# Performance work log

Measured on AMD Instinct MI355X. Metric: run time of the kernel, lower is better.

The kernel has to match this reference:

```python
import jax, jax.numpy as jnp
import numpy as np

T, B, S, D = 512, 32, 512, 512
EPS = 1e-6  # LayerNorm eps


def _ln(x, g, b):
    m = jnp.mean(x, axis=-1, keepdims=True)
    v = jnp.mean((x - m) ** 2, axis=-1, keepdims=True)
    return g * (x - m) * jax.lax.rsqrt(v + EPS) + b


def setup_inputs() -> dict:
    key = jax.random.key(0)
    ks = jax.random.split(key, 10)
    sc = 1.0 / np.sqrt(D).astype(np.float32)
    return {
        "prev_layer": jax.random.normal(ks[0], (T, B, D), jnp.float32),
        "hidden": jax.random.normal(ks[1], (B, D), jnp.float32),
        "enc_output": jax.random.normal(ks[2], (B, S, D), jnp.float32),
        "memory_length": jax.random.randint(ks[3], (B,), 1, S + 1),
        # nn.Linear weights stored as [in, out] (transposed torch layout)
        "W_in": jax.random.normal(ks[4], (D, 3 * D), jnp.float32) * sc,
        "W_enc": jax.random.normal(ks[5], (D, D), jnp.float32) * sc,
        "W_attn_in": jax.random.normal(ks[6], (D, D), jnp.float32) * sc,
        "W_hidden": jax.random.normal(ks[7], (D, D), jnp.float32) * sc,
        "W_ctx": jax.random.normal(ks[8], (D, D), jnp.float32) * sc,
        # LayerNorm gains/biases (5 LNs)
        "g_pre": jnp.ones((3 * D,), jnp.float32), "b_pre": jnp.zeros((3 * D,), jnp.float32),
        "g_enc": jnp.ones((D,), jnp.float32), "b_enc": jnp.zeros((D,), jnp.float32),
        "g_attn": jnp.ones((D,), jnp.float32), "b_attn": jnp.zeros((D,), jnp.float32),
        "g_h": jnp.ones((D,), jnp.float32), "b_h": jnp.zeros((D,), jnp.float32),
        "g_c": jnp.ones((D,), jnp.float32), "b_c": jnp.zeros((D,), jnp.float32),
    }


def reference(prev_layer, hidden, enc_output, W_in, W_enc, W_attn_in, W_hidden,
              W_ctx, g_pre, b_pre, g_enc, b_enc, g_attn, b_attn, g_h, b_h,
              g_c, b_c, memory_length):
    d = prev_layer.shape[-1]
    sqrt_d = jnp.sqrt(jnp.asarray(d, prev_layer.dtype))
    # dropout is identity in eval mode
    preact = _ln(prev_layer @ W_in, g_pre, b_pre)          # [T,B,3D]
    pctx = _ln(enc_output @ W_enc, g_enc, b_enc)           # [B,S,D]
    z, h_gate, pl_t = jnp.split(preact, 3, axis=-1)
    z = jax.nn.sigmoid(z)
    h_gate = jax.nn.sigmoid(h_gate)

    # SRU-style linear recurrence: s_t = (1-z_t)*s_{t-1} + z_t*pl_t
    def step(h, zp):
        z_t, p_t = zp
        s = (1.0 - z_t) * h + z_t * p_t
        return s, s

    hidden_last, ss = jax.lax.scan(step, hidden, (z, pl_t))  # ss: [T,B,D]

    attn_in = _ln(ss @ W_attn_in, g_attn, b_attn)            # [T,B,D]
    align = jnp.einsum('tbd,bsd->bts', attn_in, pctx)        # [B,T,S]
    mask = jnp.arange(pctx.shape[1])[None, :] < memory_length[:, None]  # [B,S]
    align = jnp.where(mask[:, None, :], align, -jnp.inf)
    av = jax.nn.softmax(align / sqrt_d, axis=-1)             # [B,T,S]
    c = jnp.einsum('bts,bsd->tbd', av, pctx)                 # [T,B,D]
    attn_out = c / sqrt_d

    trans = _ln(ss @ W_hidden, g_h, b_h) + _ln(attn_out @ W_ctx, g_c, b_c)
    out = jnp.tanh(trans)
    out = (1.0 - h_gate) * out + h_gate * prev_layer         # [T,B,D]
    p_attn = jnp.transpose(av, (1, 0, 2))                    # [T,B,S]
    return out, hidden_last, p_attn
```

## Files before the change

kernel.cpp:

```cpp
#include <hip/hip_runtime.h>
#include <hip/hip_bf16.h>
#include <cmath>

#define T_ 512
#define B_ 32
#define S_ 512
#define D_ 512
#define NCH 16
#define CT (T_ / NCH)
static constexpr float LN_EPS = 1e-6f;
static constexpr float RSQRT_D = 0.044194173824159216f;

typedef __attribute__((ext_vector_type(8))) __bf16 bf16x8;
typedef __attribute__((ext_vector_type(4))) float f32x4;

struct __align__(8) bfx4 { __hip_bfloat16 x, y, z, w; };
struct __align__(16) u16x8 { unsigned short h[8]; };

__device__ __forceinline__ void g2l16(const void* g, void* l) {
    __builtin_amdgcn_global_load_lds(
        (const __attribute__((address_space(1))) unsigned int*)g,
        (__attribute__((address_space(3))) unsigned int*)l, 16, 0, 0);
}

__device__ __forceinline__ float xr_sum16(float v) {
    v += __shfl_xor(v, 1); v += __shfl_xor(v, 2);
    v += __shfl_xor(v, 4); v += __shfl_xor(v, 8); return v;
}
__device__ __forceinline__ float xr_max16(float v) {
    v = fmaxf(v, __shfl_xor(v, 1)); v = fmaxf(v, __shfl_xor(v, 2));
    v = fmaxf(v, __shfl_xor(v, 4)); v = fmaxf(v, __shfl_xor(v, 8)); return v;
}

__device__ __forceinline__ float sigmoidf_(float x) {
    return 1.f / (1.f + __expf(-x));
}
__device__ __forceinline__ float sigmoid_fast(float x) {
    return __fdividef(1.f, 1.f + __expf(-x));
}
__device__ __forceinline__ float tanh_fast(float x) {
    return 1.f - __fdividef(2.f, __expf(2.f * x) + 1.f);
}
__device__ __forceinline__ float bfu(unsigned short u) {
    unsigned int v = ((unsigned int)u) << 16;
    return __uint_as_float(v);
}

__device__ __forceinline__ void g128_body(
    const __hip_bfloat16* __restrict__ A, long ldaE,
    const __hip_bfloat16* __restrict__ Bw,
    __hip_bfloat16* __restrict__ out, long outStrideB,
    float2* __restrict__ part, int partMul, int partBase,
    float scale, int bx, int by)
{
    __shared__ char smem[32768];
    const int m0 = by * 128, n0 = bx * 128;
    const int tid = threadIdx.x, lane = tid & 63, w = tid >> 6;
    const int wm = (w >> 1) * 64, wn = (w & 1) * 64;
    const int srow = lane >> 2, skB = (lane & 3) * 16;
    const int q = lane >> 4, c = lane & 15;

    f32x4 acc[4][4];
#pragma unroll
    for (int i = 0; i < 4; i++)
#pragma unroll
        for (int j = 0; j < 4; j++) acc[i][j] = (f32x4)(0.0f);

    const char* ga0 = (const char*)(A + (long)(m0 + w * 16 + srow) * ldaE) + skB;
    const char* ga1 = (const char*)(A + (long)(m0 + (w + 4) * 16 + srow) * ldaE) + skB;
    const char* gb0 = (const char*)(Bw + (long)(n0 + w * 16 + srow) * 512) + skB;
    const char* gb1 = (const char*)(Bw + (long)(n0 + (w + 4) * 16 + srow) * 512) + skB;
    char* la0 = smem + w * 1024 + lane * 16;
    char* la1 = smem + (w + 4) * 1024 + lane * 16;
    char* lb0 = smem + 8192 + w * 1024 + lane * 16;
    char* lb1 = smem + 8192 + (w + 4) * 1024 + lane * 16;
    const char* Ar = smem + (wm + c) * 64 + q * 16;
    const char* Br = smem + 8192 + (wn + c) * 64 + q * 16;

    g2l16(ga0, la0);
    g2l16(ga1, la1);
    g2l16(gb0, lb0);
    g2l16(gb1, lb1);
    __syncthreads();

#pragma unroll
    for (int kk = 0; kk < 16; kk++) {
        const int cb = (kk & 1) << 14;
        const int nb = cb ^ 16384;
        if (kk < 15) {
            const long kb = (long)(kk + 1) * 64;
            g2l16(ga0 + kb, la0 + nb);
            g2l16(ga1 + kb, la1 + nb);
            g2l16(gb0 + kb, lb0 + nb);
            g2l16(gb1 + kb, lb1 + nb);
        }
        bf16x8 af[4], bfr[4];
#pragma unroll
        for (int i = 0; i < 4; i++) {
            af[i] = *(const bf16x8*)(Ar + cb + i * 1024);
            bfr[i] = *(const bf16x8*)(Br + cb + i * 1024);
        }
#pragma unroll
        for (int i = 0; i < 4; i++)
#pragma unroll
            for (int j = 0; j < 4; j++)
                acc[i][j] = __builtin_amdgcn_mfma_f32_16x16x32_bf16(
                    af[i], bfr[j], acc[i][j], 0, 0, 0);
        __syncthreads();
    }

    if (part) {
        float2* sred = (float2*)smem;
#pragma unroll
        for (int i = 0; i < 4; i++)
#pragma unroll
            for (int r = 0; r < 4; r++) {
                float s = 0.f, qq = 0.f;
#pragma unroll
                for (int j = 0; j < 4; j++) {
                    float v = acc[i][j][r] * scale; s += v; qq += v * v;
                }
                s = xr_sum16(s); qq = xr_sum16(qq);
                if (c == 0) sred[(wm + i * 16 + q * 4 + r) * 2 + (w & 1)] =
                    make_float2(s, qq);
            }
        __syncthreads();
        if ((w & 1) == 0 && c == 0) {
#pragma unroll
            for (int i = 0; i < 4; i++)
#pragma unroll
                for (int r = 0; r < 4; r++) {
                    int row = wm + i * 16 + q * 4 + r;
                    float2 a = sred[row * 2], b2 = sred[row * 2 + 1];
                    part[(long)bx * 16384 + (long)(m0 + row) * partMul + partBase] =
                        make_float2(a.x + b2.x, a.y + b2.y);
                }
        }
        __syncthreads();
    }

    for (int p = 0; p < 2; p++) {
        if ((w >> 1) == p) {
#pragma unroll
            for (int i = 0; i < 4; i++)
#pragma unroll
                for (int j = 0; j < 4; j++)
#pragma unroll
                    for (int r = 0; r < 4; r++) {
                        int row = i * 16 + q * 4 + r;
                        int col = wn + j * 16 + c;
                        ((__hip_bfloat16*)smem)[row * 128 + col] =
                            __float2bfloat16(acc[i][j][r] * scale);
                    }
        }
        __syncthreads();
#pragma unroll
        for (int rnd = 0; rnd < 4; rnd++) {
            int row = rnd * 16 + (tid >> 4);
            int ch = tid & 15;
            uint4 v = *(const uint4*)(smem + row * 256 + ch * 16);
            long grow = m0 + p * 64 + row;
            *(uint4*)((char*)out + grow * outStrideB + (long)n0 * 2 + ch * 16) = v;
        }
        __syncthreads();
    }
}

__global__ __launch_bounds__(256) void g128(
    const __hip_bfloat16* __restrict__ A, long ldaE,
    const __hip_bfloat16* __restrict__ Bw, long bStrideZ,
    __hip_bfloat16* __restrict__ out, long outStrideB,
    float2* __restrict__ part, float scale, int swizzle)
{
    int bx, by, pmul = 1, pbase = 0;
    if (gridDim.z > 1) {
        bx = blockIdx.x; by = blockIdx.y;
        A += (long)blockIdx.z * 512;
        Bw += (long)blockIdx.z * bStrideZ;
        out += (long)blockIdx.z * 512;
        pmul = 32; pbase = blockIdx.z;
    } else if (swizzle) {
        const int nwg = gridDim.x * gridDim.y;
        const int lin = blockIdx.y * gridDim.x + blockIdx.x;
        const int cpx = nwg >> 3;
        const int swz = (lin & 7) * cpx + (lin >> 3);
        bx = swz % gridDim.x; by = swz / gridDim.x;
    } else { bx = blockIdx.x; by = blockIdx.y; }
    g128_body(A, ldaE, Bw, out, outStrideB, part, pmul, pbase, scale, bx, by);
}

__global__ __launch_bounds__(256) void g128mid(
    const __hip_bfloat16* __restrict__ encb,
    const __hip_bfloat16* __restrict__ ssb,
    const __hip_bfloat16* __restrict__ WE2,
    const __hip_bfloat16* __restrict__ WAH,
    __hip_bfloat16* __restrict__ E2, __hip_bfloat16* __restrict__ C2,
    float2* __restrict__ partA, float2* __restrict__ partB)
{
    const int lin = blockIdx.x;
    const int swz = (lin & 7) * 256 + (lin >> 3);
    const __hip_bfloat16 *A, *Bw;
    __hip_bfloat16* out;
    float2* part;
    int local;
    if (swz < 1024) { A = encb; Bw = WE2; out = E2; part = partA; local = swz; }
    else { A = ssb; Bw = WAH; out = C2; part = partB; local = swz - 1024; }
    const int bx = local & 7, by = local >> 3;
    g128_body(A, 512, Bw, out, 2048, part, 1, 0, 1.f, bx, by);
}

#define RC_BUF 34816
__device__ __forceinline__ void rows_core32_lds(
    const __hip_bfloat16* A, long lda,
    const __hip_bfloat16* B, long ldb,
    char* smem, f32x4 (&acc)[2][8])
{
    const int tid = threadIdx.x, lane = tid & 63, w = tid >> 6;
#pragma unroll
    for (int m = 0; m < 2; m++)
#pragma unroll
        for (int j = 0; j < 8; j++) acc[m][j] = (f32x4)(0.0f);

    const char* ga = (const char*)(A + (long)(w * 16 + (lane >> 2)) * lda) + (lane & 3) * 16;
    char* la = smem + w * 1024 + lane * 16;
    const char* gb = (const char*)(B + (long)(w * 128 + (lane >> 2)) * ldb) + (lane & 3) * 16;
    char* lb = smem + 2048 + w * 8192 + lane * 16;
    const long ldbB16 = (long)ldb * 32;
    const char* Ar = smem + (lane & 15) * 64 + (lane >> 4) * 16;
    const char* Br = smem + 2048 + (w * 128 + (lane & 15)) * 64 + (lane >> 4) * 16;

    if (w < 2) g2l16(ga, la);
#pragma unroll
    for (int s = 0; s < 8; s++) g2l16(gb + s * ldbB16, lb + s * 1024);
    __syncthreads();

#pragma unroll
    for (int kk = 0; kk < 16; kk++) {
        const int cb = (kk & 1) * RC_BUF;
        const int nb = ((kk & 1) ^ 1) * RC_BUF;
        if (kk < 15) {
            const long kb = (long)(kk + 1) * 64;
            if (w < 2) g2l16(ga + kb, la + nb);
#pragma unroll
            for (int s = 0; s < 8; s++)
                g2l16(gb + kb + s * ldbB16, lb + nb + s * 1024);
        }
        bf16x8 af[2], bfr[8];
#pragma unroll
        for (int m = 0; m < 2; m++) af[m] = *(const bf16x8*)(Ar + cb + m * 1024);
#pragma unroll
        for (int j = 0; j < 8; j++) bfr[j] = *(const bf16x8*)(Br + cb + j * 1024);
#pragma unroll
        for (int m = 0; m < 2; m++)
#pragma unroll
            for (int j = 0; j < 8; j++)
                acc[m][j] = __builtin_amdgcn_mfma_f32_16x16x32_bf16(
                    af[m], bfr[j], acc[m][j], 0, 0, 0);
        __syncthreads();
    }
}

__global__ __launch_bounds__(256, 2) void gemm_attn(
    const __hip_bfloat16* __restrict__ attninC2,
    const __hip_bfloat16* __restrict__ pctxb,
    const int* __restrict__ mlen,
    float* __restrict__ pattn, __hip_bfloat16* __restrict__ softb)
{
    __shared__ char smem[69632];
    const int b = blockIdx.z;
    const long t0 = (long)blockIdx.y * 32;
    f32x4 acc[2][8];
    rows_core32_lds(attninC2 + (long)b * 1024 + t0 * 32768, 32768,
                    pctxb + (long)b * 262144, 512, smem, acc);

    const int tid = threadIdx.x, lane = tid & 63, w = tid >> 6;
    const int q = lane >> 4, c = lane & 15;
    const int len = mlen[b];
    float* sred = (float*)smem;

#pragma unroll
    for (int m = 0; m < 2; m++)
#pragma unroll
        for (int r = 0; r < 4; r++) {
            float mx = -INFINITY;
#pragma unroll
            for (int j = 0; j < 8; j++) {
                int col = w * 128 + j * 16 + c;
                float v = acc[m][j][r] * RSQRT_D;
                acc[m][j][r] = v;
                if (col < len) mx = fmaxf(mx, v);
            }
            mx = xr_max16(mx);
            if (c == 0) sred[(m * 16 + q * 4 + r) * 4 + w] = mx;
        }
    __syncthreads();
    float rmax[2][4];
#pragma unroll
    for (int m = 0; m < 2; m++)
#pragma unroll
        for (int r = 0; r < 4; r++) {
            int row = m * 16 + q * 4 + r;
            rmax[m][r] = fmaxf(fmaxf(sred[row * 4], sred[row * 4 + 1]),
                               fmaxf(sred[row * 4 + 2], sred[row * 4 + 3]));
        }
    __syncthreads();
#pragma unroll
    for (int m = 0; m < 2; m++)
#pragma unroll
        for (int r = 0; r < 4; r++) {
            float s = 0.f;
#pragma unroll
            for (int j = 0; j < 8; j++) {
                int col = w * 128 + j * 16 + c;
                float e = (col < len) ? __expf(acc[m][j][r] - rmax[m][r]) : 0.f;
                acc[m][j][r] = e; s += e;
            }
            s = xr_sum16(s);
            if (c == 0) sred[(m * 16 + q * 4 + r) * 4 + w] = s;
        }
    __syncthreads();
    float rinv[2][4];
#pragma unroll
    for (int m = 0; m < 2; m++)
#pragma unroll
        for (int r = 0; r < 4; r++) {
            int row = m * 16 + q * 4 + r;
            rinv[m][r] = 1.f / (sred[row * 4] + sred[row * 4 + 1] +
                                sred[row * 4 + 2] + sred[row * 4 + 3]);
        }
    __syncthreads();

#pragma unroll
    for (int m = 0; m < 2; m++)
#pragma unroll
        for (int j = 0; j < 8; j++)
#pragma unroll
            for (int r = 0; r < 4; r++) {
                int row = m * 16 + q * 4 + r;
                int col = w * 128 + j * 16 + c;
                float p = acc[m][j][r] * rinv[m][r];
                acc[m][j][r] = p;
                pattn[((t0 + row) * 32 + b) * 512 + col] = p;
                ((__hip_bfloat16*)smem)[row * 512 + col] = __float2bfloat16(p);
            }
    __syncthreads();
#pragma unroll
    for (int rnd = 0; rnd < 8; rnd++) {
        int row = rnd * 4 + w;
        uint4 v = *(const uint4*)(smem + row * 1024 + lane * 16);
        *(uint4*)((char*)softb + ((t0 + row) * 32 + b) * 1024 + lane * 16) = v;
    }
}

__global__ __launch_bounds__(256) void stats4(
    const float2* __restrict__ part, float2* __restrict__ st)
{
    int r = blockIdx.x * 256 + threadIdx.x;
    float s = 0.f, qq = 0.f;
#pragma unroll
    for (int cb = 0; cb < 4; cb++) {
        float2 v = part[(long)cb * 16384 + r]; s += v.x; qq += v.y;
    }
    float m = s * (1.f / 512);
    float rs = rsqrtf(qq * (1.f / 512) - m * m + LN_EPS);
    st[r] = make_float2(m, rs);
}

__global__ __launch_bounds__(256) void ln_apply_s(
    __hip_bfloat16* __restrict__ x,
    const float2* __restrict__ st,
    const float* __restrict__ g, const float* __restrict__ bb)
{
    int i = blockIdx.x * 256 + threadIdx.x;
    int row = i >> 6;
    int c0 = (i & 63) * 8;
    float2 s = st[row];
    char* p = (char*)x + (long)row * 2048 + (long)(i & 63) * 16;
    u16x8 v = *(const u16x8*)p;
    float4 g0 = *(const float4*)(g + c0), g1 = *(const float4*)(g + c0 + 4);
    float4 b0 = *(const float4*)(bb + c0), b1 = *(const float4*)(bb + c0 + 4);
    float gv[8] = {g0.x, g0.y, g0.z, g0.w, g1.x, g1.y, g1.z, g1.w};
    float bv[8] = {b0.x, b0.y, b0.z, b0.w, b1.x, b1.y, b1.z, b1.w};
#pragma unroll
    for (int k = 0; k < 8; k++) {
        float f = (bfu(v.h[k]) - s.x) * s.y * gv[k] + bv[k];
        v.h[k] = __hip_bfloat16_raw(__float2bfloat16(f)).x;
    }
    *(u16x8*)p = v;
}

__global__ __launch_bounds__(256) void midfix(
    const __hip_bfloat16* __restrict__ E2,
    __hip_bfloat16* __restrict__ pctxb, __hip_bfloat16* __restrict__ pwT,
    const float2* __restrict__ st,
    const float* __restrict__ g, const float* __restrict__ bb,
    const float* __restrict__ uv)
{
    const int b = blockIdx.z, d0 = blockIdx.x * 32, s0 = blockIdx.y * 32;
    __shared__ __hip_bfloat16 t[32][34];
    const int tx = threadIdx.x & 31, ty = threadIdx.x >> 5;
    const float gv = g[d0 + tx], bv = bb[d0 + tx];
    const float ud = uv[d0 + tx], vd = uv[512 + d0 + tx];
#pragma unroll
    for (int i = 0; i < 4; i++) {
        int srow = s0 + ty + i * 8;
        long row = (long)b * 512 + srow;
        float2 s = st[row];
        float pc = __bfloat162float(E2[row * 1024 + d0 + tx]);
        pctxb[row * 512 + d0 + tx] =
            __float2bfloat16((pc - s.x) * s.y * gv + bv);
        float pr = __bfloat162float(E2[row * 1024 + 512 + d0 + tx]);
        t[ty + i * 8][tx] = __float2bfloat16(s.y * pr - s.y * s.x * ud + vd);
    }
    __syncthreads();
#pragma unroll
    for (int i = 0; i < 4; i++)
        pwT[(long)b * 262144 + (long)(d0 + ty + i * 8) * 512 + s0 + tx] =
            t[tx][ty + i * 8];
}

__global__ __launch_bounds__(256) void fin_ep(
    const __hip_bfloat16* __restrict__ h2r,
    const __hip_bfloat16* __restrict__ C2,
    const __hip_bfloat16* __restrict__ preb,
    const float2* __restrict__ st_c, const float2* __restrict__ st_h,
    const float2* __restrict__ st_p,
    const float* __restrict__ g_c, const float* __restrict__ b_c,
    const float* __restrict__ g_h, const float* __restrict__ b_h,
    const float* __restrict__ g_pre, const float* __restrict__ b_pre,
    const float* __restrict__ prev, float* __restrict__ out)
{
    const long m0 = (long)blockIdx.x * 32;
    const int tid = threadIdx.x;
#pragma unroll
    for (int ch = 0; ch < 16; ch++) {
        int f4 = ch * 256 + tid;
        int row = f4 >> 7;
        long rowg = m0 + row;
        int col = (f4 & 127) * 4;
        ushort4 h2 = *(const ushort4*)((const char*)h2r + rowg * 1024 + col * 2);
        ushort4 h1 = *(const ushort4*)((const char*)C2 + rowg * 2048 + 1024 + col * 2);
        ushort4 hr = *(const ushort4*)((const char*)preb + rowg * 3072 + 1024 + col * 2);
        float4 pv = *(const float4*)(prev + rowg * 512 + col);
        float4 gc = *(const float4*)(g_c + col), bc = *(const float4*)(b_c + col);
        float4 gh = *(const float4*)(g_h + col), bh = *(const float4*)(b_h + col);
        float4 gp = *(const float4*)(g_pre + 512 + col);
        float4 bp = *(const float4*)(b_pre + 512 + col);
        float2 sc = st_c[rowg], sh = st_h[rowg], sp = st_p[rowg];
        auto fuse = [&](unsigned short h2u, unsigned short h1u, unsigned short hru,
                        float pvv, float gcv, float bcv, float ghv, float bhv,
                        float gpv, float bpv) -> float {
            float t2 = (bfu(h2u) - sc.x) * sc.y * gcv + bcv;
            float t1 = (bfu(h1u) - sh.x) * sh.y * ghv + bhv;
            float hg = sigmoid_fast((bfu(hru) - sp.x) * sp.y * gpv + bpv);
            return (1.f - hg) * tanh_fast(t1 + t2) + hg * pvv;
        };
        float4 o;
        o.x = fuse(h2.x, h1.x, hr.x, pv.x, gc.x, bc.x, gh.x, bh.x, gp.x, bp.x);
        o.y = fuse(h2.y, h1.y, hr.y, pv.y, gc.y, bc.y, gh.y, bh.y, gp.y, bp.y);
        o.z = fuse(h2.z, h1.z, hr.z, pv.z, gc.z, bc.z, gh.z, bh.z, gp.z, bp.z);
        o.w = fuse(h2.w, h1.w, hr.w, pv.w, gc.w, bc.w, gh.w, bh.w, gp.w, bp.w);
        *(float4*)(out + rowg * 512 + col) = o;
    }
}

__global__ __launch_bounds__(256) void cvt4(
    const float* __restrict__ x, __hip_bfloat16* __restrict__ y, int n4)
{
    int i = blockIdx.x * 256 + threadIdx.x;
    if (i >= n4) return;
    float4 v = ((const float4*)x)[i];
    bfx4 o;
    o.x = __float2bfloat16(v.x); o.y = __float2bfloat16(v.y);
    o.z = __float2bfloat16(v.z); o.w = __float2bfloat16(v.w);
    ((bfx4*)y)[i] = o;
}

__global__ __launch_bounds__(256) void wtrans(
    const float* __restrict__ w0, const float* __restrict__ w1,
    const float* __restrict__ w2, const float* __restrict__ w3,
    const float* __restrict__ w4, __hip_bfloat16* __restrict__ WT,
    __hip_bfloat16* __restrict__ WE2)
{
    int z = blockIdx.z;
    const float* W; __hip_bfloat16* O; int N;
    if (z == 0)      { W = w0; O = WT;                          N = 1536; }
    else if (z == 1) { W = w1; O = WE2;                         N = 512; }
    else if (z == 2) { W = w2; O = WT + 786432 + 262144;        N = 512; }
    else if (z == 3) { W = w3; O = WT + 786432 + 524288;        N = 512; }
    else             { W = w4; O = WT + 786432 + 786432;        N = 512; }
    int n0 = blockIdx.x * 32, k0 = blockIdx.y * 32;
    if (n0 >= N) return;
    __shared__ float t[32][33];
    int tx = threadIdx.x & 31, ty = threadIdx.x >> 5;
#pragma unroll
    for (int i = 0; i < 4; i++)
        t[ty + i * 8][tx] = W[(long)(k0 + ty + i * 8) * N + n0 + tx];
    __syncthreads();
#pragma unroll
    for (int i = 0; i < 4; i++)
        O[(long)(n0 + ty + i * 8) * 512 + k0 + tx] =
            __float2bfloat16(t[tx][ty + i * 8]);
}

__global__ __launch_bounds__(256) void wgscale(
    const __hip_bfloat16* __restrict__ wctxT, const float* __restrict__ g,
    __hip_bfloat16* __restrict__ wgT)
{
    int i = blockIdx.x * 256 + threadIdx.x;
    int d1 = i & 511;
    wgT[i] = __float2bfloat16(__bfloat162float(wctxT[i]) * g[d1]);
}

__global__ __launch_bounds__(256) void uvk(
    const float* __restrict__ Wctx, const float* __restrict__ g,
    const float* __restrict__ b, float* __restrict__ uv)
{
    int d = blockIdx.x * 256 + threadIdx.x;
    float u = 0.f, v = 0.f;
    for (int k = 0; k < 512; k++) {
        float w = Wctx[(long)k * 512 + d];
        u += g[k] * w; v += b[k] * w;
    }
    uv[d] = u; uv[512 + d] = v;
}

__global__ __launch_bounds__(256) void stats_fin(
    const float2* __restrict__ part, float2* __restrict__ stats)
{
    int r = blockIdx.x * 256 + threadIdx.x;
    float s = 0.f, qq = 0.f;
#pragma unroll
    for (int cb = 0; cb < 12; cb++) {
        float2 v = part[(long)cb * 16384 + r]; s += v.x; qq += v.y;
    }
    float m = s * (1.f / 1536);
    float rs = rsqrtf(qq * (1.f / 1536) - m * m + LN_EPS);
    stats[r] = make_float2(m, rs);
}

__global__ __launch_bounds__(256) void scan_part1(
    const __hip_bfloat16* __restrict__ preb, const float2* __restrict__ stats,
    const float* __restrict__ gpre, const float* __restrict__ bpre,
    float* __restrict__ Ap, float* __restrict__ Bp)
{
    int i2 = blockIdx.x * 256 + threadIdx.x;
    int b = i2 >> 8, d = (i2 & 255) * 2;
    int idx = b * 512 + d;
    int ch = blockIdx.y;
    float2 gz = *(const float2*)(gpre + d), bz = *(const float2*)(bpre + d);
    float2 gp = *(const float2*)(gpre + 1024 + d);
    float2 bp = *(const float2*)(bpre + 1024 + d);
    float A0 = 1.f, s0 = 0.f, A1 = 1.f, s1 = 0.f;
    for (int t = ch * CT; t < (ch + 1) * CT; t++) {
        long row = (long)t * 32 + b;
        float2 st = stats[row];
        ushort2 zr = *(const ushort2*)(preb + row * 1536 + d);
        ushort2 pr = *(const ushort2*)(preb + row * 1536 + 1024 + d);
        float z0 = sigmoidf_((bfu(zr.x) - st.x) * st.y * gz.x + bz.x);
        float z1 = sigmoidf_((bfu(zr.y) - st.x) * st.y * gz.y + bz.y);
        float p0 = (bfu(pr.x) - st.x) * st.y * gp.x + bp.x;
        float p1 = (bfu(pr.y) - st.x) * st.y * gp.y + bp.y;
        A0 *= (1.f - z0); s0 = (1.f - z0) * s0 + z0 * p0;
        A1 *= (1.f - z1); s1 = (1.f - z1) * s1 + z1 * p1;
    }
    *(float2*)(Ap + ch * 16384 + idx) = make_float2(A0, A1);
    *(float2*)(Bp + ch * 16384 + idx) = make_float2(s0, s1);
}

__global__ __launch_bounds__(256) void scan_part2(
    const float* __restrict__ Ap, const float* __restrict__ Bp,
    const float* __restrict__ h0, float* __restrict__ sin_,
    float* __restrict__ hlast)
{
    int idx = blockIdx.x * 256 + threadIdx.x;
    float s = h0[idx];
    for (int ch = 0; ch < NCH; ch++) {
        sin_[ch * 16384 + idx] = s;
        s = Ap[ch * 16384 + idx] * s + Bp[ch * 16384 + idx];
    }
    hlast[idx] = s;
}

__global__ __launch_bounds__(256) void scan_part3(
    const __hip_bfloat16* __restrict__ preb, const float2* __restrict__ stats,
    const float* __restrict__ gpre, const float* __restrict__ bpre,
    const float* __restrict__ sin_, __hip_bfloat16* __restrict__ ssb)
{
    int i2 = blockIdx.x * 256 + threadIdx.x;
    int b = i2 >> 8, d = (i2 & 255) * 2;
    int idx = b * 512 + d;
    int ch = blockIdx.y;
    float2 gz = *(const float2*)(gpre + d), bz = *(const float2*)(bpre + d);
    float2 gp = *(const float2*)(gpre + 1024 + d);
    float2 bp = *(const float2*)(bpre + 1024 + d);
    float2 sv = *(const float2*)(sin_ + ch * 16384 + idx);
    float s0 = sv.x, s1 = sv.y;
    for (int t = ch * CT; t < (ch + 1) * CT; t++) {
        long row = (long)t * 32 + b;
        float2 st = stats[row];
        ushort2 zr = *(const ushort2*)(preb + row * 1536 + d);
        ushort2 pr = *(const ushort2*)(preb + row * 1536 + 1024 + d);
        float z0 = sigmoidf_((bfu(zr.x) - st.x) * st.y * gz.x + bz.x);
        float z1 = sigmoidf_((bfu(zr.y) - st.x) * st.y * gz.y + bz.y);
        float p0 = (bfu(pr.x) - st.x) * st.y * gp.x + bp.x;
        float p1 = (bfu(pr.y) - st.x) * st.y * gp.y + bp.y;
        s0 += z0 * (p0 - s0);
        s1 += z1 * (p1 - s1);
        ushort2 o;
        o.x = __hip_bfloat16_raw(__float2bfloat16(s0)).x;
        o.y = __hip_bfloat16_raw(__float2bfloat16(s1)).x;
        *(ushort2*)(ssb + (long)t * 16384 + idx) = o;
    }
}

extern "C" void kernel_launch(void* const* d_in, const int* in_sizes, int n_in,
                              void* d_out, int out_size, void* d_ws, size_t ws_size,
                              hipStream_t stream) {
    const float* prev  = (const float*)d_in[0];
    const float* hid0  = (const float*)d_in[1];
    const float* enc   = (const float*)d_in[2];
    const int*   mlen  = (const int*)  d_in[3];
    const float* W_in  = (const float*)d_in[4];
    const float* W_enc = (const float*)d_in[5];
    const float* W_att = (const float*)d_in[6];
    const float* W_hid = (const float*)d_in[7];
    const float* W_ctx = (const float*)d_in[8];
    const float* g_pre = (const float*)d_in[9];
    const float* b_pre = (const float*)d_in[10];
    const float* g_enc = (const float*)d_in[11];
    const float* b_enc = (const float*)d_in[12];
    const float* g_att = (const float*)d_in[13];
    const float* b_att = (const float*)d_in[14];
    const float* g_h   = (const float*)d_in[15];
    const float* b_h   = (const float*)d_in[16];
    const float* g_c   = (const float*)d_in[17];
    const float* b_c   = (const float*)d_in[18];

    float* out   = (float*)d_out;
    float* hlast = out + (long)T_ * B_ * D_;
    float* pattn = hlast + (long)B_ * D_;

    char* ws = (char*)d_ws;
    __hip_bfloat16* preb    = (__hip_bfloat16*)(ws);
    __hip_bfloat16* WT      = (__hip_bfloat16*)(ws + 50331648);
    __hip_bfloat16* prevb   = (__hip_bfloat16*)(ws + 54525952);
    __hip_bfloat16* encb    = (__hip_bfloat16*)(ws + 71303168);
    __hip_bfloat16* pctxb   = (__hip_bfloat16*)(ws + 88080384);
    __hip_bfloat16* pwT     = (__hip_bfloat16*)(ws + 104857600);
    __hip_bfloat16* ssb     = (__hip_bfloat16*)(ws + 121634816);
    __hip_bfloat16* C2      = (__hip_bfloat16*)(ws + 138412032);
    __hip_bfloat16* E2      = (__hip_bfloat16*)(ws + 171966464);
    __hip_bfloat16* softb   = (__hip_bfloat16*)(ws + 171966464);
    __hip_bfloat16* h2raw   = (__hip_bfloat16*)(ws + 188743680);
    float2* part            = (float2*)(ws + 205520896);
    float2* stats           = (float2*)(ws + 207618048);
    float* scanA            = (float*)(ws + 207749120);
    float* scanB            = (float*)(ws + 208797696);
    float* sinb             = (float*)(ws + 209846272);
    float2* stats_enc       = (float2*)(ws + 210894848);
    float2* stats_att       = (float2*)(ws + 211025920);
    float2* stats_h         = (float2*)(ws + 211156992);
    float2* stats_c         = (float2*)(ws + 211288064);
    __hip_bfloat16* WE2     = (__hip_bfloat16*)(ws + 211419136);
    float* uv               = (float*)(ws + 212467712);
    __hip_bfloat16* WgT     = (__hip_bfloat16*)scanA;
    __hip_bfloat16* Wencbf  = (__hip_bfloat16*)scanB;

    float2* partA = part;
    float2* partB = part + 8 * 16384;

    const __hip_bfloat16* W_attT = WT + 786432 + 262144;
    const __hip_bfloat16* W_ctxT = WT + 786432 + 786432;

    dim3 blk(256);

    cvt4<<<8192, blk, 0, stream>>>(prev, prevb, 2097152);
    cvt4<<<8192, blk, 0, stream>>>(enc, encb, 2097152);
    cvt4<<<256, blk, 0, stream>>>(W_enc, Wencbf, 65536);
    wtrans<<<dim3(48, 16, 5), blk, 0, stream>>>(W_in, W_enc, W_att, W_hid,
                                                W_ctx, WT, WE2);
    wgscale<<<1024, blk, 0, stream>>>(W_ctxT, g_enc, WgT);
    uvk<<<2, blk, 0, stream>>>(W_ctx, g_enc, b_enc, uv);
    g128<<<dim3(4, 4), blk, 0, stream>>>(WgT, 512, Wencbf, 0, WE2 + 262144,
                                         1024, nullptr, 1.f, 0);

    g128<<<dim3(12, 128), blk, 0, stream>>>(prevb, 512, WT, 0, preb, 3072,
                                            part, 1.f, 1);
    stats_fin<<<64, blk, 0, stream>>>(part, stats);

    scan_part1<<<dim3(32, NCH), blk, 0, stream>>>(preb, stats, g_pre, b_pre,
                                                  scanA, scanB);
    scan_part2<<<64, blk, 0, stream>>>(scanA, scanB, hid0, sinb, hlast);
    scan_part3<<<dim3(32, NCH), blk, 0, stream>>>(preb, stats, g_pre, b_pre,
                                                  sinb, ssb);

    g128mid<<<2048, blk, 0, stream>>>(encb, ssb, WE2, W_attT, E2, C2,
                                      partA, partB);
    stats4<<<64, blk, 0, stream>>>(partA, stats_enc);
    stats4<<<64, blk, 0, stream>>>(partB, stats_att);
    stats4<<<64, blk, 0, stream>>>(partB + 4 * 16384, stats_h);

    midfix<<<dim3(16, 16, 32), blk, 0, stream>>>(E2, pctxb, pwT, stats_enc,
                                                 g_enc, b_enc, uv);
    ln_apply_s<<<4096, blk, 0, stream>>>(C2, stats_att, g_att, b_att);

    gemm_attn<<<dim3(1, 16, 32), blk, 0, stream>>>(C2, pctxb, mlen,
                                                   pattn, softb);

    g128<<<dim3(4, 4, 32), blk, 0, stream>>>(softb, 16384, pwT, 262144,
                                             h2raw, 32768, part, RSQRT_D, 0);
    stats4<<<64, blk, 0, stream>>>(part, stats_c);

    fin_ep<<<512, blk, 0, stream>>>(h2raw, C2, preb, stats_c, stats_h, stats,
                                    g_c, b_c, g_h, b_h, g_pre, b_pre, prev,
                                    out);
}
```

Measured before the change: 462.3 us.

## Fuse scan phases with encoder GEMM and fold LN stats into consumers

Scan phase 1 now runs as extra blocks inside the encoder-projection GEMM launch, and scan phase 3 shares a launch with the pctx/pwT fixup kernel. The separate stats4 reductions are removed: each consumer (fixup, attention GEMM, final epilogue) sums the partial LayerNorm statistics itself. The attention-input LayerNorm is applied on the fly to A fragments inside the attention GEMM instead of in a separate pass. The goal is fewer launches and fewer full-tensor read/write passes, at the cost of extra per-fragment ALU work in the attention GEMM loop and unequal block types sharing one grid.

Result: faster. 434.6 us (-6.0%).

```diff
diff --git a/kernel.cpp b/kernel.cpp
--- a/kernel.cpp
+++ b/kernel.cpp
@@ -44,6 +44,9 @@
 __device__ __forceinline__ float bfu(unsigned short u) {
     unsigned int v = ((unsigned int)u) << 16;
     return __uint_as_float(v);
+}
+__device__ __forceinline__ unsigned short f2bu(float f) {
+    return __hip_bfloat16_raw(__float2bfloat16(f)).x;
 }
 
 __device__ __forceinline__ void g128_body(
@@ -189,43 +192,165 @@
     g128_body(A, ldaE, Bw, out, outStrideB, part, pmul, pbase, scale, bx, by);
 }
 
-__global__ __launch_bounds__(256) void g128mid(
+__global__ __launch_bounds__(256) void g128e2s(
     const __hip_bfloat16* __restrict__ encb,
-    const __hip_bfloat16* __restrict__ ssb,
     const __hip_bfloat16* __restrict__ WE2,
-    const __hip_bfloat16* __restrict__ WAH,
-    __hip_bfloat16* __restrict__ E2, __hip_bfloat16* __restrict__ C2,
-    float2* __restrict__ partA, float2* __restrict__ partB)
-{
-    const int lin = blockIdx.x;
-    const int swz = (lin & 7) * 256 + (lin >> 3);
-    const __hip_bfloat16 *A, *Bw;
-    __hip_bfloat16* out;
-    float2* part;
-    int local;
-    if (swz < 1024) { A = encb; Bw = WE2; out = E2; part = partA; local = swz; }
-    else { A = ssb; Bw = WAH; out = C2; part = partB; local = swz - 1024; }
-    const int bx = local & 7, by = local >> 3;
-    g128_body(A, 512, Bw, out, 2048, part, 1, 0, 1.f, bx, by);
+    __hip_bfloat16* __restrict__ E2, float2* __restrict__ partA,
+    const __hip_bfloat16* __restrict__ preb, const float2* __restrict__ stats,
+    const float* __restrict__ gpre, const float* __restrict__ bpre,
+    float* __restrict__ Ap, float* __restrict__ Bp)
+{
+    const int bid = blockIdx.x;
+    if (bid < 512) {
+        int i2 = (bid & 31) * 256 + threadIdx.x;
+        int b = i2 >> 8, d = (i2 & 255) * 2;
+        int idx = b * 512 + d;
+        int ch = bid >> 5;
+        float2 gz = *(const float2*)(gpre + d), bz = *(const float2*)(bpre + d);
+        float2 gp = *(const float2*)(gpre + 1024 + d);
+        float2 bp = *(const float2*)(bpre + 1024 + d);
+        float A0 = 1.f, s0 = 0.f, A1 = 1.f, s1 = 0.f;
+        for (int t = ch * CT; t < (ch + 1) * CT; t++) {
+            long row = (long)t * 32 + b;
+            float2 st = stats[row];
+            ushort2 zr = *(const ushort2*)(preb + row * 1536 + d);
+            ushort2 pr = *(const ushort2*)(preb + row * 1536 + 1024 + d);
+            float z0 = sigmoidf_((bfu(zr.x) - st.x) * st.y * gz.x + bz.x);
+            float z1 = sigmoidf_((bfu(zr.y) - st.x) * st.y * gz.y + bz.y);
+            float p0 = (bfu(pr.x) - st.x) * st.y * gp.x + bp.x;
+            float p1 = (bfu(pr.y) - st.x) * st.y * gp.y + bp.y;
+            A0 *= (1.f - z0); s0 = (1.f - z0) * s0 + z0 * p0;
+            A1 *= (1.f - z1); s1 = (1.f - z1) * s1 + z1 * p1;
+        }
+        *(float2*)(Ap + ch * 16384 + idx) = make_float2(A0, A1);
+        *(float2*)(Bp + ch * 16384 + idx) = make_float2(s0, s1);
+        return;
+    }
+    const int local = bid - 512;
+    const int swz = (local & 7) * 128 + (local >> 3);
+    g128_body(encb, 512, WE2, E2, 2048, partA, 1, 0, 1.f, swz & 7, swz >> 3);
+}
+
+__global__ __launch_bounds__(256) void mfix3(
+    const __hip_bfloat16* __restrict__ preb, const float2* __restrict__ stats,
+    const float* __restrict__ gpre, const float* __restrict__ bpre,
+    const float* __restrict__ sinb, __hip_bfloat16* __restrict__ ssb,
+    const __hip_bfloat16* __restrict__ E2,
+    __hip_bfloat16* __restrict__ pctxb, __hip_bfloat16* __restrict__ pwT,
+    const float2* __restrict__ partA,
+    const float* __restrict__ g, const float* __restrict__ bb,
+    const float* __restrict__ uv)
+{
+    __shared__ __hip_bfloat16 t[32][34];
+    __shared__ float2 sst[32];
+    const int bid = blockIdx.x;
+    if (bid < 512) {
+        int i2 = (bid & 31) * 256 + threadIdx.x;
+        int b = i2 >> 8, d = (i2 & 255) * 2;
+        int idx = b * 512 + d;
+        int ch = bid >> 5;
+        float2 gz = *(const float2*)(gpre + d), bz = *(const float2*)(bpre + d);
+        float2 gp = *(const float2*)(gpre + 1024 + d);
+        float2 bp = *(const float2*)(bpre + 1024 + d);
+        float2 sv = *(const float2*)(sinb + ch * 16384 + idx);
+        float s0 = sv.x, s1 = sv.y;
+        for (int tt = ch * CT; tt < (ch + 1) * CT; tt++) {
+            long row = (long)tt * 32 + b;
+            float2 st = stats[row];
+            ushort2 zr = *(const ushort2*)(preb + row * 1536 + d);
+            ushort2 pr = *(const ushort2*)(preb + row * 1536 + 1024 + d);
+            float z0 = sigmoidf_((bfu(zr.x) - st.x) * st.y * gz.x + bz.x);
+            float z1 = sigmoidf_((bfu(zr.y) - st.x) * st.y * gz.y + bz.y);
+            float p0 = (bfu(pr.x) - st.x) * st.y * gp.x + bp.x;
+            float p1 = (bfu(pr.y) - st.x) * st.y * gp.y + bp.y;
+            s0 += z0 * (p0 - s0);
+            s1 += z1 * (p1 - s1);
+            ushort2 o;
+            o.x = f2bu(s0); o.y = f2bu(s1);
+            *(ushort2*)(ssb + (long)tt * 16384 + idx) = o;
+        }
+        return;
+    }
+    const int local = bid - 512;
+    const int d0 = (local & 15) * 32;
+    const int s0 = ((local >> 4) & 15) * 32;
+    const int b = local >> 8;
+    if (threadIdx.x < 32) {
+        long row = (long)b * 512 + s0 + threadIdx.x;
+        float s = 0.f, qq = 0.f;
+#pragma unroll
+        for (int cb = 0; cb < 4; cb++) {
+            float2 v = partA[(long)cb * 16384 + row]; s += v.x; qq += v.y;
+        }
+        float mn = s * (1.f / 512);
+        sst[threadIdx.x] =
+            make_float2(mn, rsqrtf(qq * (1.f / 512) - mn * mn + LN_EPS));
+    }
+    __syncthreads();
+    const int tx = threadIdx.x & 31, ty = threadIdx.x >> 5;
+    const float gv = g[d0 + tx], bv = bb[d0 + tx];
+    const float ud = uv[d0 + tx], vd = uv[512 + d0 + tx];
+#pragma unroll
+    for (int i = 0; i < 4; i++) {
+        int srow = s0 + ty + i * 8;
+        long row = (long)b * 512 + srow;
+        float2 s = sst[ty + i * 8];
+        float pc = __bfloat162float(E2[row * 1024 + d0 + tx]);
+        pctxb[row * 512 + d0 + tx] =
+            __float2bfloat16((pc - s.x) * s.y * gv + bv);
+        float pr = __bfloat162float(E2[row * 1024 + 512 + d0 + tx]);
+        t[ty + i * 8][tx] = __float2bfloat16(s.y * pr - s.y * s.x * ud + vd);
+    }
+    __syncthreads();
+#pragma unroll
+    for (int i = 0; i < 4; i++)
+        pwT[(long)b * 262144 + (long)(d0 + ty + i * 8) * 512 + s0 + tx] =
+            t[tx][ty + i * 8];
 }
 
 #define RC_BUF 34816
-__device__ __forceinline__ void rows_core32_lds(
-    const __hip_bfloat16* A, long lda,
-    const __hip_bfloat16* B, long ldb,
-    char* smem, f32x4 (&acc)[2][8])
-{
+__global__ __launch_bounds__(256, 2) void gemm_attn(
+    const __hip_bfloat16* __restrict__ attninC2,
+    const __hip_bfloat16* __restrict__ pctxb,
+    const float2* __restrict__ partB,
+    const float* __restrict__ g_att, const float* __restrict__ b_att,
+    const int* __restrict__ mlen,
+    float* __restrict__ pattn, __hip_bfloat16* __restrict__ softb)
+{
+    __shared__ char smem[74240];
+    float2* sst = (float2*)(smem + 69632);
+    float* gln = (float*)(smem + 69888);
+    float* bln = (float*)(smem + 71936);
+    const int b = blockIdx.z;
+    const long t0 = (long)blockIdx.y * 32;
     const int tid = threadIdx.x, lane = tid & 63, w = tid >> 6;
+
+    if (tid < 32) {
+        long grow = (t0 + tid) * 32 + b;
+        float s = 0.f, qq = 0.f;
+#pragma unroll
+        for (int cb = 0; cb < 4; cb++) {
+            float2 v = partB[(long)cb * 16384 + grow]; s += v.x; qq += v.y;
+        }
+        float mn = s * (1.f / 512);
+        sst[tid] = make_float2(mn, rsqrtf(qq * (1.f / 512) - mn * mn + LN_EPS));
+    }
+    gln[tid] = g_att[tid]; gln[256 + tid] = g_att[256 + tid];
+    bln[tid] = b_att[tid]; bln[256 + tid] = b_att[256 + tid];
+
+    f32x4 acc[2][8];
 #pragma unroll
     for (int m = 0; m < 2; m++)
 #pragma unroll
         for (int j = 0; j < 8; j++) acc[m][j] = (f32x4)(0.0f);
 
-    const char* ga = (const char*)(A + (long)(w * 16 + (lane >> 2)) * lda) + (lane & 3) * 16;
+    const __hip_bfloat16* A = attninC2 + (long)b * 1024 + t0 * 32768;
+    const __hip_bfloat16* Bm = pctxb + (long)b * 262144;
+    const char* ga = (const char*)(A + (long)(w * 16 + (lane >> 2)) * 32768) + (lane & 3) * 16;
     char* la = smem + w * 1024 + lane * 16;
-    const char* gb = (const char*)(B + (long)(w * 128 + (lane >> 2)) * ldb) + (lane & 3) * 16;
+    const char* gb = (const char*)(Bm + (long)(w * 128 + (lane >> 2)) * 512) + (lane & 3) * 16;
     char* lb = smem + 2048 + w * 8192 + lane * 16;
-    const long ldbB16 = (long)ldb * 32;
+    const long ldbB16 = 512L * 32;
     const char* Ar = smem + (lane & 15) * 64 + (lane >> 4) * 16;
     const char* Br = smem + 2048 + (w * 128 + (lane & 15)) * 64 + (lane >> 4) * 16;
 
@@ -233,6 +358,9 @@
 #pragma unroll
     for (int s = 0; s < 8; s++) g2l16(gb + s * ldbB16, lb + s * 1024);
     __syncthreads();
+
+    const int fr = lane & 15, kq = lane >> 4;
+    const float2 st0 = sst[fr], st1 = sst[16 + fr];
 
 #pragma unroll
     for (int kk = 0; kk < 16; kk++) {
@@ -250,6 +378,24 @@
         for (int m = 0; m < 2; m++) af[m] = *(const bf16x8*)(Ar + cb + m * 1024);
 #pragma unroll
         for (int j = 0; j < 8; j++) bfr[j] = *(const bf16x8*)(Br + cb + j * 1024);
+        {
+            const int k0 = kk * 32 + kq * 8;
+            float4 gq0 = *(const float4*)(gln + k0);
+            float4 gq1 = *(const float4*)(gln + k0 + 4);
+            float4 bq0 = *(const float4*)(bln + k0);
+            float4 bq1 = *(const float4*)(bln + k0 + 4);
+            float gj[8] = {gq0.x, gq0.y, gq0.z, gq0.w, gq1.x, gq1.y, gq1.z, gq1.w};
+            float bj[8] = {bq0.x, bq0.y, bq0.z, bq0.w, bq1.x, bq1.y, bq1.z, bq1.w};
+            u16x8 u0 = __builtin_bit_cast(u16x8, af[0]);
+            u16x8 u1 = __builtin_bit_cast(u16x8, af[1]);
+#pragma unroll
+            for (int j = 0; j < 8; j++) {
+                u0.h[j] = f2bu((bfu(u0.h[j]) - st0.x) * st0.y * gj[j] + bj[j]);
+                u1.h[j] = f2bu((bfu(u1.h[j]) - st1.x) * st1.y * gj[j] + bj[j]);
+            }
+            af[0] = __builtin_bit_cast(bf16x8, u0);
+            af[1] = __builtin_bit_cast(bf16x8, u1);
+        }
 #pragma unroll
         for (int m = 0; m < 2; m++)
 #pragma unroll
@@ -258,22 +404,7 @@
                     af[m], bfr[j], acc[m][j], 0, 0, 0);
         __syncthreads();
     }
-}
-
-__global__ __launch_bounds__(256, 2) void gemm_attn(
-    const __hip_bfloat16* __restrict__ attninC2,
-    const __hip_bfloat16* __restrict__ pctxb,
-    const int* __restrict__ mlen,
-    float* __restrict__ pattn, __hip_bfloat16* __restrict__ softb)
-{
-    __shared__ char smem[69632];
-    const int b = blockIdx.z;
-    const long t0 = (long)blockIdx.y * 32;
-    f32x4 acc[2][8];
-    rows_core32_lds(attninC2 + (long)b * 1024 + t0 * 32768, 32768,
-                    pctxb + (long)b * 262144, 512, smem, acc);
-
-    const int tid = threadIdx.x, lane = tid & 63, w = tid >> 6;
+
     const int q = lane >> 4, c = lane & 15;
     const int len = mlen[b];
     float* sred = (float*)smem;
@@ -339,7 +470,6 @@
                 int row = m * 16 + q * 4 + r;
                 int col = w * 128 + j * 16 + c;
                 float p = acc[m][j][r] * rinv[m][r];
-                acc[m][j][r] = p;
                 pattn[((t0 + row) * 32 + b) * 512 + col] = p;
                 ((__hip_bfloat16*)smem)[row * 512 + col] = __float2bfloat16(p);
             }
@@ -352,86 +482,41 @@
     }
 }
 
-__global__ __launch_bounds__(256) void stats4(
-    const float2* __restrict__ part, float2* __restrict__ st)
-{
-    int r = blockIdx.x * 256 + threadIdx.x;
-    float s = 0.f, qq = 0.f;
-#pragma unroll
-    for (int cb = 0; cb < 4; cb++) {
-        float2 v = part[(long)cb * 16384 + r]; s += v.x; qq += v.y;
-    }
-    float m = s * (1.f / 512);
-    float rs = rsqrtf(qq * (1.f / 512) - m * m + LN_EPS);
-    st[r] = make_float2(m, rs);
-}
-
-__global__ __launch_bounds__(256) void ln_apply_s(
-    __hip_bfloat16* __restrict__ x,
-    const float2* __restrict__ st,
-    const float* __restrict__ g, const float* __restrict__ bb)
-{
-    int i = blockIdx.x * 256 + threadIdx.x;
-    int row = i >> 6;
-    int c0 = (i & 63) * 8;
-    float2 s = st[row];
-    char* p = (char*)x + (long)row * 2048 + (long)(i & 63) * 16;
-    u16x8 v = *(const u16x8*)p;
-    float4 g0 = *(const float4*)(g + c0), g1 = *(const float4*)(g + c0 + 4);
-    float4 b0 = *(const float4*)(bb + c0), b1 = *(const float4*)(bb + c0 + 4);
-    float gv[8] = {g0.x, g0.y, g0.z, g0.w, g1.x, g1.y, g1.z, g1.w};
-    float bv[8] = {b0.x, b0.y, b0.z, b0.w, b1.x, b1.y, b1.z, b1.w};
-#pragma unroll
-    for (int k = 0; k < 8; k++) {
-        float f = (bfu(v.h[k]) - s.x) * s.y * gv[k] + bv[k];
-        v.h[k] = __hip_bfloat16_raw(__float2bfloat16(f)).x;
-    }
-    *(u16x8*)p = v;
-}
-
-__global__ __launch_bounds__(256) void midfix(
-    const __hip_bfloat16* __restrict__ E2,
-    __hip_bfloat16* __restrict__ pctxb, __hip_bfloat16* __restrict__ pwT,
-    const float2* __restrict__ st,
-    const float* __restrict__ g, const float* __restrict__ bb,
-    const float* __restrict__ uv)
-{
-    const int b = blockIdx.z, d0 = blockIdx.x * 32, s0 = blockIdx.y * 32;
-    __shared__ __hip_bfloat16 t[32][34];
-    const int tx = threadIdx.x & 31, ty = threadIdx.x >> 5;
-    const float gv = g[d0 + tx], bv = bb[d0 + tx];
-    const float ud = uv[d0 + tx], vd = uv[512 + d0 + tx];
-#pragma unroll
-    for (int i = 0; i < 4; i++) {
-        int srow = s0 + ty + i * 8;
-        long row = (long)b * 512 + srow;
-        float2 s = st[row];
-        float pc = __bfloat162float(E2[row * 1024 + d0 + tx]);
-        pctxb[row * 512 + d0 + tx] =
-            __float2bfloat16((pc - s.x) * s.y * gv + bv);
-        float pr = __bfloat162float(E2[row * 1024 + 512 + d0 + tx]);
-        t[ty + i * 8][tx] = __float2bfloat16(s.y * pr - s.y * s.x * ud + vd);
-    }
-    __syncthreads();
-#pragma unroll
-    for (int i = 0; i < 4; i++)
-        pwT[(long)b * 262144 + (long)(d0 + ty + i * 8) * 512 + s0 + tx] =
-            t[tx][ty + i * 8];
-}
-
 __global__ __launch_bounds__(256) void fin_ep(
     const __hip_bfloat16* __restrict__ h2r,
     const __hip_bfloat16* __restrict__ C2,
     const __hip_bfloat16* __restrict__ preb,
-    const float2* __restrict__ st_c, const float2* __restrict__ st_h,
+    const float2* __restrict__ partC,
+    const float2* __restrict__ partH,
     const float2* __restrict__ st_p,
     const float* __restrict__ g_c, const float* __restrict__ b_c,
     const float* __restrict__ g_h, const float* __restrict__ b_h,
     const float* __restrict__ g_pre, const float* __restrict__ b_pre,
     const float* __restrict__ prev, float* __restrict__ out)
 {
+    __shared__ float2 shc[32], shh[32];
     const long m0 = (long)blockIdx.x * 32;
     const int tid = threadIdx.x;
+    if (tid < 32) {
+        long rowg = m0 + tid;
+        float s = 0.f, qq = 0.f;
+#pragma unroll
+        for (int cb = 0; cb < 4; cb++) {
+            float2 v = partC[(long)cb * 16384 + rowg]; s += v.x; qq += v.y;
+        }
+        float mn = s * (1.f / 512);
+        shc[tid] = make_float2(mn, rsqrtf(qq * (1.f / 512) - mn * mn + LN_EPS));
+    } else if (tid < 64) {
+        long rowg = m0 + tid - 32;
+        float s = 0.f, qq = 0.f;
+#pragma unroll
+        for (int cb = 0; cb < 4; cb++) {
+            float2 v = partH[(long)cb * 16384 + rowg]; s += v.x; qq += v.y;
+        }
+        float mn = s * (1.f / 512);
+        shh[tid - 32] = make_float2(mn, rsqrtf(qq * (1.f / 512) - mn * mn + LN_EPS));
+    }
+    __syncthreads();
 #pragma unroll
     for (int ch = 0; ch < 16; ch++) {
         int f4 = ch * 256 + tid;
@@ -446,7 +531,7 @@
         float4 gh = *(const float4*)(g_h + col), bh = *(const float4*)(b_h + col);
         float4 gp = *(const float4*)(g_pre + 512 + col);
         float4 bp = *(const float4*)(b_pre + 512 + col);
-        float2 sc = st_c[rowg], sh = st_h[rowg], sp = st_p[rowg];
+        float2 sc = shc[row], sh = shh[row], sp = st_p[rowg];
         auto fuse = [&](unsigned short h2u, unsigned short h1u, unsigned short hru,
                         float pvv, float gcv, float bcv, float ghv, float bhv,
                         float gpv, float bpv) -> float {
@@ -539,35 +624,6 @@
     stats[r] = make_float2(m, rs);
 }
 
-__global__ __launch_bounds__(256) void scan_part1(
-    const __hip_bfloat16* __restrict__ preb, const float2* __restrict__ stats,
-    const float* __restrict__ gpre, const float* __restrict__ bpre,
-    float* __restrict__ Ap, float* __restrict__ Bp)
-{
-    int i2 = blockIdx.x * 256 + threadIdx.x;
-    int b = i2 >> 8, d = (i2 & 255) * 2;
-    int idx = b * 512 + d;
-    int ch = blockIdx.y;
-    float2 gz = *(const float2*)(gpre + d), bz = *(const float2*)(bpre + d);
-    float2 gp = *(const float2*)(gpre + 1024 + d);
-    float2 bp = *(const float2*)(bpre + 1024 + d);
-    float A0 = 1.f, s0 = 0.f, A1 = 1.f, s1 = 0.f;
-    for (int t = ch * CT; t < (ch + 1) * CT; t++) {
-        long row = (long)t * 32 + b;
-        float2 st = stats[row];
-        ushort2 zr = *(const ushort2*)(preb + row * 1536 + d);
-        ushort2 pr = *(const ushort2*)(preb + row * 1536 + 1024 + d);
-        float z0 = sigmoidf_((bfu(zr.x) - st.x) * st.y * gz.x + bz.x);
-        float z1 = sigmoidf_((bfu(zr.y) - st.x) * st.y * gz.y + bz.y);
-        float p0 = (bfu(pr.x) - st.x) * st.y * gp.x + bp.x;
-        float p1 = (bfu(pr.y) - st.x) * st.y * gp.y + bp.y;
-        A0 *= (1.f - z0); s0 = (1.f - z0) * s0 + z0 * p0;
-        A1 *= (1.f - z1); s1 = (1.f - z1) * s1 + z1 * p1;
-    }
-    *(float2*)(Ap + ch * 16384 + idx) = make_float2(A0, A1);
-    *(float2*)(Bp + ch * 16384 + idx) = make_float2(s0, s1);
-}
-
 __global__ __launch_bounds__(256) void scan_part2(
     const float* __restrict__ Ap, const float* __restrict__ Bp,
     const float* __restrict__ h0, float* __restrict__ sin_,
@@ -580,38 +636,6 @@
         s = Ap[ch * 16384 + idx] * s + Bp[ch * 16384 + idx];
     }
     hlast[idx] = s;
-}
-
-__global__ __launch_bounds__(256) void scan_part3(
-    const __hip_bfloat16* __restrict__ preb, const float2* __restrict__ stats,
-    const float* __restrict__ gpre, const float* __restrict__ bpre,
-    const float* __restrict__ sin_, __hip_bfloat16* __restrict__ ssb)
-{
-    int i2 = blockIdx.x * 256 + threadIdx.x;
-    int b = i2 >> 8, d = (i2 & 255) * 2;
-    int idx = b * 512 + d;
-    int ch = blockIdx.y;
-    float2 gz = *(const float2*)(gpre + d), bz = *(const float2*)(bpre + d);
-    float2 gp = *(const float2*)(gpre + 1024 + d);
-    float2 bp = *(const float2*)(bpre + 1024 + d);
-    float2 sv = *(const float2*)(sin_ + ch * 16384 + idx);
-    float s0 = sv.x, s1 = sv.y;
-    for (int t = ch * CT; t < (ch + 1) * CT; t++) {
-        long row = (long)t * 32 + b;
-        float2 st = stats[row];
-        ushort2 zr = *(const ushort2*)(preb + row * 1536 + d);
-        ushort2 pr = *(const ushort2*)(preb + row * 1536 + 1024 + d);
-        float z0 = sigmoidf_((bfu(zr.x) - st.x) * st.y * gz.x + bz.x);
-        float z1 = sigmoidf_((bfu(zr.y) - st.x) * st.y * gz.y + bz.y);
-        float p0 = (bfu(pr.x) - st.x) * st.y * gp.x + bp.x;
-        float p1 = (bfu(pr.y) - st.x) * st.y * gp.y + bp.y;
-        s0 += z0 * (p0 - s0);
-        s1 += z1 * (p1 - s1);
-        ushort2 o;
-        o.x = __hip_bfloat16_raw(__float2bfloat16(s0)).x;
-        o.y = __hip_bfloat16_raw(__float2bfloat16(s1)).x;
-        *(ushort2*)(ssb + (long)t * 16384 + idx) = o;
-    }
 }
 
 extern "C" void kernel_launch(void* const* d_in, const int* in_sizes, int n_in,
@@ -658,10 +682,6 @@
     float* scanA            = (float*)(ws + 207749120);
     float* scanB            = (float*)(ws + 208797696);
     float* sinb             = (float*)(ws + 209846272);
-    float2* stats_enc       = (float2*)(ws + 210894848);
-    float2* stats_att       = (float2*)(ws + 211025920);
-    float2* stats_h         = (float2*)(ws + 211156992);
-    float2* stats_c         = (float2*)(ws + 211288064);
     __hip_bfloat16* WE2     = (__hip_bfloat16*)(ws + 211419136);
     float* uv               = (float*)(ws + 212467712);
     __hip_bfloat16* WgT     = (__hip_bfloat16*)scanA;
@@ -669,6 +689,7 @@
 
     float2* partA = part;
     float2* partB = part + 8 * 16384;
+    float2* partC = part;
 
     const __hip_bfloat16* W_attT = WT + 786432 + 262144;
     const __hip_bfloat16* W_ctxT = WT + 786432 + 786432;
@@ -689,30 +710,25 @@
                                             part, 1.f, 1);
     stats_fin<<<64, blk, 0, stream>>>(part, stats);
 
-    scan_part1<<<dim3(32, NCH), blk, 0, stream>>>(preb, stats, g_pre, b_pre,
-                                                  scanA, scanB);
+    g128e2s<<<1536, blk, 0, stream>>>(encb, WE2, E2, partA, preb, stats,
+                                      g_pre, b_pre, scanA, scanB);
     scan_part2<<<64, blk, 0, stream>>>(scanA, scanB, hid0, sinb, hlast);
-    scan_part3<<<dim3(32, NCH), blk, 0, stream>>>(preb, stats, g_pre, b_pre,
-                                                  sinb, ssb);
-
-    g128mid<<<2048, blk, 0, stream>>>(encb, ssb, WE2, W_attT, E2, C2,
-                                      partA, partB);
-    stats4<<<64, blk, 0, stream>>>(partA, stats_enc);
-    stats4<<<64, blk, 0, stream>>>(partB, stats_att);
-    stats4<<<64, blk, 0, stream>>>(partB + 4 * 16384, stats_h);
-
-    midfix<<<dim3(16, 16, 32), blk, 0, stream>>>(E2, pctxb, pwT, stats_enc,
-                                                 g_enc, b_enc, uv);
-    ln_apply_s<<<4096, blk, 0, stream>>>(C2, stats_att, g_att, b_att);
-
-    gemm_attn<<<dim3(1, 16, 32), blk, 0, stream>>>(C2, pctxb, mlen,
+
+    mfix3<<<8704, blk, 0, stream>>>(preb, stats, g_pre, b_pre, sinb, ssb,
+                                    E2, pctxb, pwT, partA, g_enc, b_enc, uv);
+
+    g128<<<dim3(8, 128), blk, 0, stream>>>(ssb, 512, W_attT, 0, C2, 2048,
+                                           partB, 1.f, 1);
+
+    gemm_attn<<<dim3(1, 16, 32), blk, 0, stream>>>(C2, pctxb, partB,
+                                                   g_att, b_att, mlen,
                                                    pattn, softb);
 
     g128<<<dim3(4, 4, 32), blk, 0, stream>>>(softb, 16384, pwT, 262144,
-                                             h2raw, 32768, part, RSQRT_D, 0);
-    stats4<<<64, blk, 0, stream>>>(part, stats_c);
-
-    fin_ep<<<512, blk, 0, stream>>>(h2raw, C2, preb, stats_c, stats_h, stats,
+                                             h2raw, 32768, partC, RSQRT_D, 0);
+
+    fin_ep<<<512, blk, 0, stream>>>(h2raw, C2, preb, partC,
+                                    partB + 4 * 16384, stats,
                                     g_c, b_c, g_h, b_h, g_pre, b_pre, prev,
                                     out);
 }
```
